# Kernel optimization log

Measured on AMD Instinct MI355X. Metric: run time of the kernel, lower is better.

The kernel has to match this reference:

```python
import jax, jax.numpy as jnp
import numpy as np

N_NODES = 100000
N_EDGES = 500000
N_REL = 6
IN_DIM = 64
HID = 128
HEADS = 4
C = HID // HEADS  # 32 per-head channels
N_GRAPHS = 1024
EPS = 1e-16


def setup_inputs() -> dict:
    key = jax.random.key(0)
    ks = jax.random.split(key, 20)
    x = jax.random.normal(ks[0], (N_NODES, IN_DIM), dtype=jnp.float32)
    edge_index = jax.random.randint(ks[1], (N_REL, 2, N_EDGES), 0, N_NODES, dtype=jnp.int64)
    batch = jnp.sort(jax.random.randint(ks[2], (N_NODES,), 0, N_GRAPHS, dtype=jnp.int64))
    s = 0.02
    return {
        "x": x, "edge_index": edge_index, "batch": batch,
        # layer1 GAT params (stacked over 6 relations)
        "W1": jax.random.normal(ks[3], (N_REL, IN_DIM, HID), dtype=jnp.float32) * s,
        "as1": jax.random.normal(ks[4], (N_REL, HEADS, C), dtype=jnp.float32) * s,
        "ad1": jax.random.normal(ks[5], (N_REL, HEADS, C), dtype=jnp.float32) * s,
        "b1": jnp.zeros((N_REL, HID), dtype=jnp.float32),
        # layer2 GAT params
        "W2": jax.random.normal(ks[6], (N_REL, HID, HID), dtype=jnp.float32) * s,
        "as2": jax.random.normal(ks[7], (N_REL, HEADS, C), dtype=jnp.float32) * s,
        "ad2": jax.random.normal(ks[8], (N_REL, HEADS, C), dtype=jnp.float32) * s,
        "b2": jnp.zeros((N_REL, HID), dtype=jnp.float32),
        # layernorms
        "g1": jnp.ones((HID,), dtype=jnp.float32), "be1": jnp.zeros((HID,), dtype=jnp.float32),
        "g2": jnp.ones((HID,), dtype=jnp.float32), "be2": jnp.zeros((HID,), dtype=jnp.float32),
        # attention pooling query + output proj
        "q": jax.random.normal(ks[9], (HID,), dtype=jnp.float32) * s,
        "Wp": jax.random.normal(ks[10], (HID, HID), dtype=jnp.float32) * s,
        "bp": jnp.zeros((HID,), dtype=jnp.float32),
    }


def _gat_hetero_layer(x, edge_index, W, a_src, a_dst, b):
    # HeteroConv(aggr='sum') over R GATConv relations, add_self_loops=False, eval (no dropout)
    N = x.shape[0]
    out = jnp.zeros((N, HEADS * C), dtype=x.dtype)
    for r in range(N_REL):
        h = (x @ W[r]).reshape(N, HEADS, C)          # [N,H,C]
        al_s = (h * a_src[r]).sum(-1)                # [N,H]
        al_d = (h * a_dst[r]).sum(-1)                # [N,H]
        src, dst = edge_index[r, 0], edge_index[r, 1]
        e = jax.nn.leaky_relu(al_s[src] + al_d[dst], 0.2)   # [E,H]
        m = jax.ops.segment_max(e, dst, num_segments=N)
        ex = jnp.exp(e - m[dst])
        den = jax.ops.segment_sum(ex, dst, num_segments=N)
        alpha = ex / (den[dst] + EPS)                # segment softmax over incoming edges
        msg = h[src] * alpha[:, :, None]             # [E,H,C]
        agg = jax.ops.segment_sum(msg, dst, num_segments=N).reshape(N, HEADS * C)
        out = out + agg + b[r]
    return out


def _layernorm(x, g, b):
    mu = x.mean(-1, keepdims=True)
    v = ((x - mu) ** 2).mean(-1, keepdims=True)
    return (x - mu) * jax.lax.rsqrt(v + 1e-5) * g + b


def _softsign(x):
    return x / (1.0 + jnp.abs(x))


def reference(x, edge_index, batch, W1, as1, ad1, b1, W2, as2, ad2, b2,
              g1, be1, g2, be2, q, Wp, bp):
    h = _gat_hetero_layer(x, edge_index, W1, as1, ad1, b1)
    h = _layernorm(_softsign(h), g1, be1)
    h = _gat_hetero_layer(h, edge_index, W2, as2, ad2, b2)
    h = _layernorm(_softsign(h), g2, be2)
    # attention pooling: segment softmax over batch, then weighted scatter-sum
    scores = (h * q).sum(-1)                                   # [N]
    m = jax.ops.segment_max(scores, batch, num_segments=N_GRAPHS)
    ex = jnp.exp(scores - m[batch])
    den = jax.ops.segment_sum(ex, batch, num_segments=N_GRAPHS)
    w = ex / (den[batch] + EPS)
    pooled = jax.ops.segment_sum(h * w[:, None], batch, num_segments=N_GRAPHS)  # [G,HID]
    return pooled @ Wp + bp
```

## Files before the change

kernel.cpp:

```cpp
#include <hip/hip_runtime.h>
#include <hip/hip_bf16.h>
#include <hip/hip_fp16.h>

#define N_NODES_C 100000
#define N_EDGES_C 500000
#define N_REL_C 6
#define IN_DIM_C 64
#define HID_C 128
#define HEADS_C 4
#define CPH_C 32
#define N_GRAPHS_C 1024
#define NBLK_SCAN 391

typedef _Float16 f16x8 __attribute__((ext_vector_type(8)));
typedef float f32x4 __attribute__((ext_vector_type(4)));

__global__ __launch_bounds__(256) void hist_rank_kernel(const int* __restrict__ ei,
                                                        int* __restrict__ cnt,
                                                        int* __restrict__ rank) {
    int i = blockIdx.x * 256 + threadIdx.x;
    if (i >= N_REL_C * N_EDGES_C) return;
    int r = i / N_EDGES_C;
    int e = i - r * N_EDGES_C;
    int dst = ei[(size_t)r * 2 * N_EDGES_C + N_EDGES_C + e];
    rank[i] = atomicAdd(&cnt[r * N_NODES_C + dst], 1);
}

__global__ __launch_bounds__(256) void scan1_kernel(const int* __restrict__ cnt,
                                                    int* __restrict__ rowptr,
                                                    int* __restrict__ blocksums) {
    int r = blockIdx.y, b = blockIdx.x, t = threadIdx.x;
    int idx = b * 256 + t;
    int v = (idx < N_NODES_C) ? cnt[r * N_NODES_C + idx] : 0;
    int orig = v;
    int lane = t & 63, w = t >> 6;
#pragma unroll
    for (int off = 1; off < 64; off <<= 1) {
        int n = __shfl_up(v, off);
        if (lane >= off) v += n;
    }
    __shared__ int wt[4];
    if (lane == 63) wt[w] = v;
    __syncthreads();
    int add = 0;
    for (int i = 0; i < w; i++) add += wt[i];
    v += add;
    if (idx < N_NODES_C) rowptr[(size_t)r * (N_NODES_C + 1) + idx] = v - orig;
    if (t == 255) blocksums[r * NBLK_SCAN + b] = v;
}

__global__ __launch_bounds__(512) void scan2_kernel(int* __restrict__ blocksums) {
    int r = blockIdx.x, t = threadIdx.x;
    int v = (t < NBLK_SCAN) ? blocksums[r * NBLK_SCAN + t] : 0;
    int orig = v;
    int lane = t & 63, w = t >> 6;
#pragma unroll
    for (int off = 1; off < 64; off <<= 1) {
        int n = __shfl_up(v, off);
        if (lane >= off) v += n;
    }
    __shared__ int wt[8];
    if (lane == 63) wt[w] = v;
    __syncthreads();
    int add = 0;
    for (int i = 0; i < w; i++) add += wt[i];
    v += add;
    if (t < NBLK_SCAN) blocksums[r * NBLK_SCAN + t] = v - orig;
}

__global__ __launch_bounds__(256) void scan3_kernel(int* __restrict__ rowptr,
                                                    const int* __restrict__ blocksums) {
    int r = blockIdx.y, b = blockIdx.x, t = threadIdx.x;
    int idx = b * 256 + t;
    if (idx < N_NODES_C) {
        rowptr[(size_t)r * (N_NODES_C + 1) + idx] += blocksums[r * NBLK_SCAN + b];
    }
    if (b == 0 && t == 0) rowptr[(size_t)r * (N_NODES_C + 1) + N_NODES_C] = N_EDGES_C;
}

__global__ __launch_bounds__(256) void scatter_kernel(const int* __restrict__ ei,
                                                      const int* __restrict__ rowptr,
                                                      const int* __restrict__ rank,
                                                      int* __restrict__ srcids) {
    int i = blockIdx.x * 256 + threadIdx.x;
    if (i >= N_REL_C * N_EDGES_C) return;
    int r = i / N_EDGES_C;
    int e = i - r * N_EDGES_C;
    int src = ei[(size_t)r * 2 * N_EDGES_C + e];
    int dst = ei[(size_t)r * 2 * N_EDGES_C + N_EDGES_C + e];
    int pos = rowptr[(size_t)r * (N_NODES_C + 1) + dst] + rank[i];
    srcids[(size_t)r * N_EDGES_C + pos] = src;
}

__global__ __launch_bounds__(256) void convert_all_kernel(const float* __restrict__ x,
                                                          __half* __restrict__ xh,
                                                          const float* __restrict__ W1,
                                                          const float* __restrict__ W2,
                                                          __half* __restrict__ Wt1,
                                                          __half* __restrict__ Wt2) {
    int i = blockIdx.x * 256 + threadIdx.x;
    if (i < N_NODES_C * IN_DIM_C / 4) {
        float4 v = ((const float4*)x)[i];
        union { __half h[4]; uint2 u; } u;
        u.h[0] = __float2half(v.x); u.h[1] = __float2half(v.y);
        u.h[2] = __float2half(v.z); u.h[3] = __float2half(v.w);
        ((uint2*)xh)[i] = u.u;
    }
    if (i < N_REL_C * IN_DIM_C * HID_C) {
        int r = i / (IN_DIM_C * HID_C);
        int rem = i - r * (IN_DIM_C * HID_C);
        int k = rem / HID_C, n = rem - k * HID_C;
        Wt1[(size_t)r * HID_C * IN_DIM_C + n * IN_DIM_C + k] = __float2half(W1[i]);
    }
    if (i < N_REL_C * HID_C * HID_C) {
        int r = i / (HID_C * HID_C);
        int rem = i - r * (HID_C * HID_C);
        int k = rem / HID_C, n = rem - k * HID_C;
        Wt2[(size_t)r * HID_C * HID_C + n * HID_C + k] = __float2half(W2[i]);
    }
}

template <int K>
__global__ __launch_bounds__(256) void gemm_mfma_kernel(
    const __half* __restrict__ Xh, const __half* __restrict__ Wtbase,
    __half* __restrict__ Hbase,
    const float* __restrict__ asbase, const float* __restrict__ adbase,
    float* __restrict__ alsbase, float* __restrict__ aldbase) {
    __shared__ _Float16 sh[4][16][HID_C];
    const int slot = blockIdx.y;
    const __half* Wt = Wtbase + (size_t)slot * HID_C * K;
    __half* H = Hbase + (size_t)slot * N_NODES_C * HID_C;
    const int wave = threadIdx.x >> 6, lane = threadIdx.x & 63;
    const int r0 = blockIdx.x * 64 + wave * 16;
    const int m = lane & 15, quad = lane >> 4;
    int arow = r0 + m;
    if (arow > N_NODES_C - 1) arow = N_NODES_C - 1;
    const __half* ap = Xh + (size_t)arow * K + quad * 8;
    const __half* bp = Wt + (size_t)m * K + quad * 8;

    f32x4 acc[8];
#pragma unroll
    for (int t = 0; t < 8; t++) acc[t] = (f32x4){0.f, 0.f, 0.f, 0.f};

#pragma unroll
    for (int kc = 0; kc < K; kc += 32) {
        f16x8 a = *(const f16x8*)(ap + kc);
#pragma unroll
        for (int t = 0; t < 8; t++) {
            f16x8 b = *(const f16x8*)(bp + (size_t)t * 16 * K + kc);
            acc[t] = __builtin_amdgcn_mfma_f32_16x16x32_f16(a, b, acc[t], 0, 0, 0);
        }
    }

#pragma unroll
    for (int t = 0; t < 8; t++)
#pragma unroll
        for (int i = 0; i < 4; i++)
            sh[wave][quad * 4 + i][t * 16 + m] = (_Float16)acc[t][i];
#pragma unroll
    for (int p = 0; p < 4; p++) {
        int idx = p * 512 + lane * 8;
        int row = idx >> 7;
        int col = idx & 127;
        int R = r0 + row;
        if (R < N_NODES_C)
            *(uint4*)(H + (size_t)R * HID_C + col) = *(const uint4*)&sh[wave][row][col];
    }

    const float* a_s = asbase + slot * HID_C;
    const float* a_d = adbase + slot * HID_C;
    float* als = alsbase + (size_t)slot * N_NODES_C * HEADS_C;
    float* ald = aldbase + (size_t)slot * N_NODES_C * HEADS_C;
    float ps[4][4], pd[4][4];
#pragma unroll
    for (int h = 0; h < 4; h++) {
        float as0 = a_s[h * 32 + m], as1 = a_s[h * 32 + 16 + m];
        float ad0 = a_d[h * 32 + m], ad1 = a_d[h * 32 + 16 + m];
#pragma unroll
        for (int i = 0; i < 4; i++) {
            ps[h][i] = acc[2 * h][i] * as0 + acc[2 * h + 1][i] * as1;
            pd[h][i] = acc[2 * h][i] * ad0 + acc[2 * h + 1][i] * ad1;
        }
    }
#pragma unroll
    for (int off = 1; off < 16; off <<= 1) {
#pragma unroll
        for (int h = 0; h < 4; h++)
#pragma unroll
            for (int i = 0; i < 4; i++) {
                ps[h][i] += __shfl_xor(ps[h][i], off);
                pd[h][i] += __shfl_xor(pd[h][i], off);
            }
    }
#pragma unroll
    for (int h = 0; h < 4; h++) {
        if (m == h) {
#pragma unroll
            for (int i = 0; i < 4; i++) {
                int R = r0 + quad * 4 + i;
                if (R < N_NODES_C) {
                    als[R * HEADS_C + h] = ps[h][i];
                    ald[R * HEADS_C + h] = pd[h][i];
                }
            }
        }
    }
}

__global__ __launch_bounds__(256) void csr_agg_kernel(
    const int* __restrict__ rowptr, const int* __restrict__ srcids,
    const __half* __restrict__ A, const float* __restrict__ als,
    const float* __restrict__ ald, int rel_start, int rel_cnt,
    const float* __restrict__ bias, int first, int last,
    float* __restrict__ B,
    const float* __restrict__ g, const float* __restrict__ be,
    __half* __restrict__ Cbh) {
    int node = blockIdx.x * 4 + (threadIdx.x >> 6);
    int lane = threadIdx.x & 63;
    int grp = lane >> 4;
    int j16 = lane & 15;
    int head = j16 >> 2;
    int cbase = j16 * 8;

    float acc[8];
    if (first) {
#pragma unroll
        for (int t = 0; t < 8; t++) {
            float s = 0.f;
#pragma unroll
            for (int r = 0; r < N_REL_C; r++) s += bias[r * HID_C + cbase + t];
            acc[t] = s;
        }
    } else {
        float4 b0 = *(const float4*)(B + (size_t)node * HID_C + cbase);
        float4 b1 = *(const float4*)(B + (size_t)node * HID_C + cbase + 4);
        acc[0] = b0.x; acc[1] = b0.y; acc[2] = b0.z; acc[3] = b0.w;
        acc[4] = b1.x; acc[5] = b1.y; acc[6] = b1.z; acc[7] = b1.w;
    }

    for (int j = 0; j < rel_cnt; j++) {
        int r = rel_start + j;
        const int* rp = rowptr + (size_t)r * (N_NODES_C + 1);
        const int* sp = srcids + (size_t)r * N_EDGES_C;
        const __half* Aj = A + (size_t)j * N_NODES_C * HID_C;
        const float* alj = als + (size_t)j * N_NODES_C * HEADS_C;
        float aldv = ald[(size_t)j * N_NODES_C * HEADS_C + node * HEADS_C + head];
        int s = rp[node], e = rp[node + 1];
        float racc[8];
#pragma unroll
        for (int t = 0; t < 8; t++) racc[t] = 0.f;
        float rden = 0.f;

        union HU { uint4 u; _Float16 h[8]; };
        int i = s + grp;
        int src = (i < e) ? sp[i] : 0;
        HU rw; rw.u = *(const uint4*)(Aj + (size_t)src * HID_C + cbase);
        float lg = alj[src * HEADS_C + head];
        for (; i < e; i += 4) {
            int nsrc = (i + 4 < e) ? sp[i + 4] : 0;
            HU nrw; nrw.u = *(const uint4*)(Aj + (size_t)nsrc * HID_C + cbase);
            float nlg = alj[nsrc * HEADS_C + head];
            float v = lg + aldv;
            v = fmaxf(v, 0.2f * v);
            float ex = __expf(v);
            rden += ex;
#pragma unroll
            for (int t = 0; t < 8; t++)
                racc[t] = fmaf((float)rw.h[t], ex, racc[t]);
            src = nsrc; rw = nrw; lg = nlg;
        }
#pragma unroll
        for (int off = 16; off < 64; off <<= 1) {
            rden += __shfl_xor(rden, off);
#pragma unroll
            for (int t = 0; t < 8; t++) racc[t] += __shfl_xor(racc[t], off);
        }
        float inv = 1.f / (rden + 1e-16f);
#pragma unroll
        for (int t = 0; t < 8; t++) acc[t] = fmaf(racc[t], inv, acc[t]);
    }

    if (!last) {
        if (grp == 0) {
            float4 o0 = make_float4(acc[0], acc[1], acc[2], acc[3]);
            float4 o1 = make_float4(acc[4], acc[5], acc[6], acc[7]);
            *(float4*)(B + (size_t)node * HID_C + cbase) = o0;
            *(float4*)(B + (size_t)node * HID_C + cbase + 4) = o1;
        }
    } else {
        float ss[8];
        float sum = 0.f, sq = 0.f;
#pragma unroll
        for (int t = 0; t < 8; t++) {
            float v = acc[t] / (1.f + fabsf(acc[t]));
            ss[t] = v;
            sum += v;
            sq = fmaf(v, v, sq);
        }
#pragma unroll
        for (int off = 1; off < 16; off <<= 1) {
            sum += __shfl_xor(sum, off);
            sq += __shfl_xor(sq, off);
        }
        float mu = sum * (1.f / 128.f);
        float var = sq * (1.f / 128.f) - mu * mu;
        float inv = rsqrtf(var + 1e-5f);
        if (grp == 0) {
            float4 gv0 = *(const float4*)(g + cbase);
            float4 gv1 = *(const float4*)(g + cbase + 4);
            float4 bv0 = *(const float4*)(be + cbase);
            float4 bv1 = *(const float4*)(be + cbase + 4);
            union { uint4 u; __half2 h2[4]; } ow;
            ow.h2[0] = __float22half2_rn(make_float2(
                (ss[0] - mu) * inv * gv0.x + bv0.x, (ss[1] - mu) * inv * gv0.y + bv0.y));
            ow.h2[1] = __float22half2_rn(make_float2(
                (ss[2] - mu) * inv * gv0.z + bv0.z, (ss[3] - mu) * inv * gv0.w + bv0.w));
            ow.h2[2] = __float22half2_rn(make_float2(
                (ss[4] - mu) * inv * gv1.x + bv1.x, (ss[5] - mu) * inv * gv1.y + bv1.y));
            ow.h2[3] = __float22half2_rn(make_float2(
                (ss[6] - mu) * inv * gv1.z + bv1.z, (ss[7] - mu) * inv * gv1.w + bv1.w));
            *(uint4*)(Cbh + (size_t)node * HID_C + cbase) = ow.u;
        }
    }
}

__device__ __forceinline__ int lower_bound_i(const int* __restrict__ a, int n, int v) {
    int lo = 0, hi = n;
    while (lo < hi) {
        int mid = (lo + hi) >> 1;
        if (a[mid] < v) lo = mid + 1; else hi = mid;
    }
    return lo;
}

__global__ __launch_bounds__(256) void pool_kernel(const __half* __restrict__ H,
                                                   const int* __restrict__ batch,
                                                   const float* __restrict__ q,
                                                   float* __restrict__ pooled) {
    int g = blockIdx.x;
    int t = threadIdx.x;
    int wave = t >> 6, lane = t & 63;
    int start = lower_bound_i(batch, N_NODES_C, g);
    int end = lower_bound_i(batch, N_NODES_C, g + 1);
    float q0 = q[lane * 2], q1 = q[lane * 2 + 1];
    float p0 = 0.f, p1 = 0.f, den = 0.f;
    for (int n = start + wave; n < end; n += 4) {
        float2 hv = __half22float2(*(const __half2*)(H + (size_t)n * HID_C + lane * 2));
        float part = hv.x * q0 + hv.y * q1;
#pragma unroll
        for (int off = 1; off < 64; off <<= 1) part += __shfl_xor(part, off);
        float exs = __expf(part);
        den += exs;
        p0 = fmaf(exs, hv.x, p0);
        p1 = fmaf(exs, hv.y, p1);
    }
    __shared__ float sp[4][HID_C];
    __shared__ float sden[4];
    sp[wave][lane * 2] = p0;
    sp[wave][lane * 2 + 1] = p1;
    if (lane == 0) sden[wave] = den;
    __syncthreads();
    if (wave == 0) {
        float a0 = sp[0][lane * 2] + sp[1][lane * 2] + sp[2][lane * 2] + sp[3][lane * 2];
        float a1 = sp[0][lane * 2 + 1] + sp[1][lane * 2 + 1] + sp[2][lane * 2 + 1] + sp[3][lane * 2 + 1];
        float d = sden[0] + sden[1] + sden[2] + sden[3];
        float w = 1.f / (d + 1e-16f);
        pooled[(size_t)g * HID_C + lane * 2] = a0 * w;
        pooled[(size_t)g * HID_C + lane * 2 + 1] = a1 * w;
    }
}

__global__ __launch_bounds__(128) void proj_kernel(const float* __restrict__ pooled,
                                                   const float* __restrict__ Wp,
                                                   const float* __restrict__ bp,
                                                   float* __restrict__ out) {
    int g = blockIdx.x, c = threadIdx.x;
    __shared__ float pl[HID_C];
    pl[c] = pooled[(size_t)g * HID_C + c];
    __syncthreads();
    float s = bp[c];
    for (int k = 0; k < HID_C; k++) s = fmaf(pl[k], Wp[k * HID_C + c], s);
    out[(size_t)g * HID_C + c] = s;
}

extern "C" void kernel_launch(void* const* d_in, const int* in_sizes, int n_in,
                              void* d_out, int out_size, void* d_ws, size_t ws_size,
                              hipStream_t stream) {
    const float* x   = (const float*)d_in[0];
    const int* ei    = (const int*)d_in[1];
    const int* batch = (const int*)d_in[2];
    const float* W1  = (const float*)d_in[3];
    const float* as1 = (const float*)d_in[4];
    const float* ad1 = (const float*)d_in[5];
    const float* b1  = (const float*)d_in[6];
    const float* W2  = (const float*)d_in[7];
    const float* as2 = (const float*)d_in[8];
    const float* ad2 = (const float*)d_in[9];
    const float* b2  = (const float*)d_in[10];
    const float* g1  = (const float*)d_in[11];
    const float* be1 = (const float*)d_in[12];
    const float* g2  = (const float*)d_in[13];
    const float* be2 = (const float*)d_in[14];
    const float* q   = (const float*)d_in[15];
    const float* Wp  = (const float*)d_in[16];
    const float* bp  = (const float*)d_in[17];
    float* out = (float*)d_out;

    const size_t NH = (size_t)N_NODES_C * HID_C;
    char* w = (char*)d_ws;
    __half* xh    = (__half*)w;   w += (size_t)N_NODES_C * IN_DIM_C * 2;
    __half* Cbh   = (__half*)w;   w += NH * 2;
    __half* Wt1   = (__half*)w;   w += (size_t)N_REL_C * IN_DIM_C * HID_C * 2;
    __half* Wt2   = (__half*)w;   w += (size_t)N_REL_C * HID_C * HID_C * 2;
    float* pooled = (float*)w;    w += (size_t)N_GRAPHS_C * HID_C * 4;
    int* rowptr   = (int*)w;      w += ((size_t)N_REL_C * (N_NODES_C + 1) * 4 + 15) & ~15ull;
    int* srcids   = (int*)w;      w += (size_t)N_REL_C * N_EDGES_C * 4;
    int* cnt      = (int*)w;      w += (size_t)N_REL_C * N_NODES_C * 4;
    int* bsums    = (int*)w;      w += ((size_t)N_REL_C * NBLK_SCAN * 4 + 15) & ~15ull;

    const size_t fixed_bytes = (size_t)(w - (char*)d_ws);
    const size_t slot_bytes = NH * 2 + 2 * (size_t)N_NODES_C * HEADS_C * 4;
    int nA = 1;
    float* B = nullptr;
    {
        size_t rem = (ws_size > fixed_bytes) ? (ws_size - fixed_bytes) : 0;
        size_t k = rem / slot_bytes;
        if (k >= 6) {
            nA = 6;
        } else {
            size_t rem2 = (rem > NH * 4) ? (rem - NH * 4) : 0;
            size_t k2 = rem2 / slot_bytes;
            nA = (int)(k2 < 1 ? 1 : (k2 > 5 ? 5 : k2));
        }
    }
    float* als = (float*)w;
    float* ald = als + (size_t)nA * N_NODES_C * HEADS_C;
    __half* A  = (__half*)(ald + (size_t)nA * N_NODES_C * HEADS_C);
    if (nA < 6) B = (float*)(A + (size_t)nA * NH);
    int* rank = (int*)A;

    hipMemsetAsync(cnt, 0, (size_t)N_REL_C * N_NODES_C * sizeof(int), stream);
    const int ehg = (N_REL_C * N_EDGES_C + 255) / 256;
    hist_rank_kernel<<<ehg, 256, 0, stream>>>(ei, cnt, rank);
    scan1_kernel<<<dim3(NBLK_SCAN, N_REL_C), 256, 0, stream>>>(cnt, rowptr, bsums);
    scan2_kernel<<<N_REL_C, 512, 0, stream>>>(bsums);
    scan3_kernel<<<dim3(NBLK_SCAN, N_REL_C), 256, 0, stream>>>(rowptr, bsums);
    scatter_kernel<<<ehg, 256, 0, stream>>>(ei, rowptr, rank, srcids);

    convert_all_kernel<<<(N_NODES_C * IN_DIM_C / 4 + 255) / 256, 256, 0, stream>>>(
        x, xh, W1, W2, Wt1, Wt2);

    const int gemm_grid = (N_NODES_C + 63) / 64;
    const int agg_grid = N_NODES_C / 4;

    for (int gs = 0; gs < N_REL_C; gs += nA) {
        int c2 = (N_REL_C - gs) < nA ? (N_REL_C - gs) : nA;
        gemm_mfma_kernel<IN_DIM_C><<<dim3(gemm_grid, c2), 256, 0, stream>>>(
            xh, Wt1 + (size_t)gs * IN_DIM_C * HID_C, A,
            as1 + gs * HID_C, ad1 + gs * HID_C, als, ald);
        csr_agg_kernel<<<agg_grid, 256, 0, stream>>>(
            rowptr, srcids, A, als, ald, gs, c2,
            b1, (gs == 0) ? 1 : 0, (gs + c2 == N_REL_C) ? 1 : 0,
            B, g1, be1, Cbh);
    }
    for (int gs = 0; gs < N_REL_C; gs += nA) {
        int c2 = (N_REL_C - gs) < nA ? (N_REL_C - gs) : nA;
        gemm_mfma_kernel<HID_C><<<dim3(gemm_grid, c2), 256, 0, stream>>>(
            Cbh, Wt2 + (size_t)gs * HID_C * HID_C, A,
            as2 + gs * HID_C, ad2 + gs * HID_C, als, ald);
        csr_agg_kernel<<<agg_grid, 256, 0, stream>>>(
            rowptr, srcids, A, als, ald, gs, c2,
            b2, (gs == 0) ? 1 : 0, (gs + c2 == N_REL_C) ? 1 : 0,
            B, g2, be2, Cbh);
    }

    pool_kernel<<<N_GRAPHS_C, 256, 0, stream>>>(Cbh, batch, q, pooled);
    proj_kernel<<<N_GRAPHS_C, 128, 0, stream>>>(pooled, Wp, bp, out);
}
```

Before: 1.045 ms.

## Drop scan3 pass and reuse A fragments across relations in GEMM

```diff
diff --git a/kernel.cpp b/kernel.cpp
--- a/kernel.cpp
+++ b/kernel.cpp
@@ -68,18 +68,9 @@
     if (t < NBLK_SCAN) blocksums[r * NBLK_SCAN + t] = v - orig;
 }
 
-__global__ __launch_bounds__(256) void scan3_kernel(int* __restrict__ rowptr,
-                                                    const int* __restrict__ blocksums) {
-    int r = blockIdx.y, b = blockIdx.x, t = threadIdx.x;
-    int idx = b * 256 + t;
-    if (idx < N_NODES_C) {
-        rowptr[(size_t)r * (N_NODES_C + 1) + idx] += blocksums[r * NBLK_SCAN + b];
-    }
-    if (b == 0 && t == 0) rowptr[(size_t)r * (N_NODES_C + 1) + N_NODES_C] = N_EDGES_C;
-}
-
 __global__ __launch_bounds__(256) void scatter_kernel(const int* __restrict__ ei,
-                                                      const int* __restrict__ rowptr,
+                                                      const int* __restrict__ rowptrP,
+                                                      const int* __restrict__ bsums,
                                                       const int* __restrict__ rank,
                                                       int* __restrict__ srcids) {
     int i = blockIdx.x * 256 + threadIdx.x;
@@ -88,8 +79,8 @@
     int e = i - r * N_EDGES_C;
     int src = ei[(size_t)r * 2 * N_EDGES_C + e];
     int dst = ei[(size_t)r * 2 * N_EDGES_C + N_EDGES_C + e];
-    int pos = rowptr[(size_t)r * (N_NODES_C + 1) + dst] + rank[i];
-    srcids[(size_t)r * N_EDGES_C + pos] = src;
+    int base = rowptrP[(size_t)r * (N_NODES_C + 1) + dst] + bsums[r * NBLK_SCAN + (dst >> 8)];
+    srcids[(size_t)r * N_EDGES_C + base + rank[i]] = src;
 }
 
 __global__ __launch_bounds__(256) void convert_all_kernel(const float* __restrict__ x,
@@ -123,84 +114,89 @@
 template <int K>
 __global__ __launch_bounds__(256) void gemm_mfma_kernel(
     const __half* __restrict__ Xh, const __half* __restrict__ Wtbase,
-    __half* __restrict__ Hbase,
+    __half* __restrict__ Hbase, int rel_start, int rel_cnt,
     const float* __restrict__ asbase, const float* __restrict__ adbase,
     float* __restrict__ alsbase, float* __restrict__ aldbase) {
     __shared__ _Float16 sh[4][16][HID_C];
-    const int slot = blockIdx.y;
-    const __half* Wt = Wtbase + (size_t)slot * HID_C * K;
-    __half* H = Hbase + (size_t)slot * N_NODES_C * HID_C;
     const int wave = threadIdx.x >> 6, lane = threadIdx.x & 63;
     const int r0 = blockIdx.x * 64 + wave * 16;
     const int m = lane & 15, quad = lane >> 4;
     int arow = r0 + m;
     if (arow > N_NODES_C - 1) arow = N_NODES_C - 1;
-    const __half* ap = Xh + (size_t)arow * K + quad * 8;
-    const __half* bp = Wt + (size_t)m * K + quad * 8;
-
-    f32x4 acc[8];
-#pragma unroll
-    for (int t = 0; t < 8; t++) acc[t] = (f32x4){0.f, 0.f, 0.f, 0.f};
-
-#pragma unroll
-    for (int kc = 0; kc < K; kc += 32) {
-        f16x8 a = *(const f16x8*)(ap + kc);
-#pragma unroll
-        for (int t = 0; t < 8; t++) {
-            f16x8 b = *(const f16x8*)(bp + (size_t)t * 16 * K + kc);
-            acc[t] = __builtin_amdgcn_mfma_f32_16x16x32_f16(a, b, acc[t], 0, 0, 0);
-        }
-    }
-
-#pragma unroll
-    for (int t = 0; t < 8; t++)
-#pragma unroll
-        for (int i = 0; i < 4; i++)
-            sh[wave][quad * 4 + i][t * 16 + m] = (_Float16)acc[t][i];
-#pragma unroll
-    for (int p = 0; p < 4; p++) {
-        int idx = p * 512 + lane * 8;
-        int row = idx >> 7;
-        int col = idx & 127;
-        int R = r0 + row;
-        if (R < N_NODES_C)
-            *(uint4*)(H + (size_t)R * HID_C + col) = *(const uint4*)&sh[wave][row][col];
-    }
-
-    const float* a_s = asbase + slot * HID_C;
-    const float* a_d = adbase + slot * HID_C;
-    float* als = alsbase + (size_t)slot * N_NODES_C * HEADS_C;
-    float* ald = aldbase + (size_t)slot * N_NODES_C * HEADS_C;
-    float ps[4][4], pd[4][4];
-#pragma unroll
-    for (int h = 0; h < 4; h++) {
-        float as0 = a_s[h * 32 + m], as1 = a_s[h * 32 + 16 + m];
-        float ad0 = a_d[h * 32 + m], ad1 = a_d[h * 32 + 16 + m];
-#pragma unroll
-        for (int i = 0; i < 4; i++) {
-            ps[h][i] = acc[2 * h][i] * as0 + acc[2 * h + 1][i] * as1;
-            pd[h][i] = acc[2 * h][i] * ad0 + acc[2 * h + 1][i] * ad1;
-        }
-    }
-#pragma unroll
-    for (int off = 1; off < 16; off <<= 1) {
-#pragma unroll
-        for (int h = 0; h < 4; h++)
+
+    f16x8 afrag[K / 32];
+#pragma unroll
+    for (int kc = 0; kc < K; kc += 32)
+        afrag[kc / 32] = *(const f16x8*)(Xh + (size_t)arow * K + quad * 8 + kc);
+
+    for (int j = 0; j < rel_cnt; j++) {
+        int slot = rel_start + j;
+        const __half* Wt = Wtbase + (size_t)slot * HID_C * K;
+        __half* H = Hbase + (size_t)j * N_NODES_C * HID_C;
+        const __half* bp = Wt + (size_t)m * K + quad * 8;
+
+        f32x4 acc[8];
+#pragma unroll
+        for (int t = 0; t < 8; t++) acc[t] = (f32x4){0.f, 0.f, 0.f, 0.f};
+#pragma unroll
+        for (int kc = 0; kc < K; kc += 32) {
+#pragma unroll
+            for (int t = 0; t < 8; t++) {
+                f16x8 b = *(const f16x8*)(bp + (size_t)t * 16 * K + kc);
+                acc[t] = __builtin_amdgcn_mfma_f32_16x16x32_f16(afrag[kc / 32], b, acc[t], 0, 0, 0);
+            }
+        }
+
+#pragma unroll
+        for (int t = 0; t < 8; t++)
+#pragma unroll
+            for (int i = 0; i < 4; i++)
+                sh[wave][quad * 4 + i][t * 16 + m] = (_Float16)acc[t][i];
+#pragma unroll
+        for (int p = 0; p < 4; p++) {
+            int idx = p * 512 + lane * 8;
+            int row = idx >> 7;
+            int col = idx & 127;
+            int R = r0 + row;
+            if (R < N_NODES_C)
+                *(uint4*)(H + (size_t)R * HID_C + col) = *(const uint4*)&sh[wave][row][col];
+        }
+
+        const float* a_s = asbase + slot * HID_C;
+        const float* a_d = adbase + slot * HID_C;
+        float* als = alsbase + (size_t)j * N_NODES_C * HEADS_C;
+        float* ald = aldbase + (size_t)j * N_NODES_C * HEADS_C;
+        float ps[4][4], pd[4][4];
+#pragma unroll
+        for (int h = 0; h < 4; h++) {
+            float as0 = a_s[h * 32 + m], as1 = a_s[h * 32 + 16 + m];
+            float ad0 = a_d[h * 32 + m], ad1 = a_d[h * 32 + 16 + m];
 #pragma unroll
             for (int i = 0; i < 4; i++) {
-                ps[h][i] += __shfl_xor(ps[h][i], off);
-                pd[h][i] += __shfl_xor(pd[h][i], off);
+                ps[h][i] = acc[2 * h][i] * as0 + acc[2 * h + 1][i] * as1;
+                pd[h][i] = acc[2 * h][i] * ad0 + acc[2 * h + 1][i] * ad1;
             }
-    }
-#pragma unroll
-    for (int h = 0; h < 4; h++) {
-        if (m == h) {
-#pragma unroll
-            for (int i = 0; i < 4; i++) {
-                int R = r0 + quad * 4 + i;
-                if (R < N_NODES_C) {
-                    als[R * HEADS_C + h] = ps[h][i];
-                    ald[R * HEADS_C + h] = pd[h][i];
+        }
+#pragma unroll
+        for (int off = 1; off < 16; off <<= 1) {
+#pragma unroll
+            for (int h = 0; h < 4; h++)
+#pragma unroll
+                for (int i = 0; i < 4; i++) {
+                    ps[h][i] += __shfl_xor(ps[h][i], off);
+                    pd[h][i] += __shfl_xor(pd[h][i], off);
+                }
+        }
+#pragma unroll
+        for (int h = 0; h < 4; h++) {
+            if (m == h) {
+#pragma unroll
+                for (int i = 0; i < 4; i++) {
+                    int R = r0 + quad * 4 + i;
+                    if (R < N_NODES_C) {
+                        als[R * HEADS_C + h] = ps[h][i];
+                        ald[R * HEADS_C + h] = pd[h][i];
+                    }
                 }
             }
         }
@@ -208,7 +204,8 @@
 }
 
 __global__ __launch_bounds__(256) void csr_agg_kernel(
-    const int* __restrict__ rowptr, const int* __restrict__ srcids,
+    const int* __restrict__ rowptrP, const int* __restrict__ bsums,
+    const int* __restrict__ srcids,
     const __half* __restrict__ A, const float* __restrict__ als,
     const float* __restrict__ ald, int rel_start, int rel_cnt,
     const float* __restrict__ bias, int first, int last,
@@ -240,12 +237,15 @@
 
     for (int j = 0; j < rel_cnt; j++) {
         int r = rel_start + j;
-        const int* rp = rowptr + (size_t)r * (N_NODES_C + 1);
+        const int* rp = rowptrP + (size_t)r * (N_NODES_C + 1);
+        const int* bs = bsums + r * NBLK_SCAN;
         const int* sp = srcids + (size_t)r * N_EDGES_C;
         const __half* Aj = A + (size_t)j * N_NODES_C * HID_C;
         const float* alj = als + (size_t)j * N_NODES_C * HEADS_C;
         float aldv = ald[(size_t)j * N_NODES_C * HEADS_C + node * HEADS_C + head];
-        int s = rp[node], e = rp[node + 1];
+        int s = rp[node] + bs[node >> 8];
+        int e = (node == N_NODES_C - 1) ? N_EDGES_C
+                                        : rp[node + 1] + bs[(node + 1) >> 8];
         float racc[8];
 #pragma unroll
         for (int t = 0; t < 8; t++) racc[t] = 0.f;
@@ -444,8 +444,7 @@
     hist_rank_kernel<<<ehg, 256, 0, stream>>>(ei, cnt, rank);
     scan1_kernel<<<dim3(NBLK_SCAN, N_REL_C), 256, 0, stream>>>(cnt, rowptr, bsums);
     scan2_kernel<<<N_REL_C, 512, 0, stream>>>(bsums);
-    scan3_kernel<<<dim3(NBLK_SCAN, N_REL_C), 256, 0, stream>>>(rowptr, bsums);
-    scatter_kernel<<<ehg, 256, 0, stream>>>(ei, rowptr, rank, srcids);
+    scatter_kernel<<<ehg, 256, 0, stream>>>(ei, rowptr, bsums, rank, srcids);
 
     convert_all_kernel<<<(N_NODES_C * IN_DIM_C / 4 + 255) / 256, 256, 0, stream>>>(
         x, xh, W1, W2, Wt1, Wt2);
@@ -455,21 +454,19 @@
 
     for (int gs = 0; gs < N_REL_C; gs += nA) {
         int c2 = (N_REL_C - gs) < nA ? (N_REL_C - gs) : nA;
-        gemm_mfma_kernel<IN_DIM_C><<<dim3(gemm_grid, c2), 256, 0, stream>>>(
-            xh, Wt1 + (size_t)gs * IN_DIM_C * HID_C, A,
-            as1 + gs * HID_C, ad1 + gs * HID_C, als, ald);
+        gemm_mfma_kernel<IN_DIM_C><<<gemm_grid, 256, 0, stream>>>(
+            xh, Wt1, A, gs, c2, as1, ad1, als, ald);
         csr_agg_kernel<<<agg_grid, 256, 0, stream>>>(
-            rowptr, srcids, A, als, ald, gs, c2,
+            rowptr, bsums, srcids, A, als, ald, gs, c2,
             b1, (gs == 0) ? 1 : 0, (gs + c2 == N_REL_C) ? 1 : 0,
             B, g1, be1, Cbh);
     }
     for (int gs = 0; gs < N_REL_C; gs += nA) {
         int c2 = (N_REL_C - gs) < nA ? (N_REL_C - gs) : nA;
-        gemm_mfma_kernel<HID_C><<<dim3(gemm_grid, c2), 256, 0, stream>>>(
-            Cbh, Wt2 + (size_t)gs * HID_C * HID_C, A,
-            as2 + gs * HID_C, ad2 + gs * HID_C, als, ald);
+        gemm_mfma_kernel<HID_C><<<gemm_grid, 256, 0, stream>>>(
+            Cbh, Wt2, A, gs, c2, as2, ad2, als, ald);
         csr_agg_kernel<<<agg_grid, 256, 0, stream>>>(
-            rowptr, srcids, A, als, ald, gs, c2,
+            rowptr, bsums, srcids, A, als, ald, gs, c2,
             b2, (gs == 0) ? 1 : 0, (gs + c2 == N_REL_C) ? 1 : 0,
             B, g2, be2, Cbh);
     }
```

Measured after the change: 1.079 ms. 3.3% more time.
